# Kernel optimization log

Measured on AMD Instinct MI355X. Metric: run time of the kernel, lower is better.

The kernel has to match this reference:

```python
import jax, jax.numpy as jnp
import numpy as np

NUM_HEADS = 4
EPS = 1e-12  # torch F.normalize eps


def conv1x1(x, w):
    # x: (b,c,h,w), w: (co,ci,1,1) -> pointwise conv == channel GEMM
    return jnp.einsum('bchw,dc->bdhw', x, w[:, :, 0, 0])


def dwconv3x3(x, w):
    # depthwise 3x3, groups = channels; w: (c,1,3,3)
    c = x.shape[1]
    return jax.lax.conv_general_dilated(
        x, w, window_strides=(1, 1), padding=((1, 1), (1, 1)),
        dimension_numbers=('NCHW', 'OIHW', 'NCHW'), feature_group_count=c)


def l2_normalize(x, axis=-1):
    n = jnp.sqrt(jnp.sum(x * x, axis=axis, keepdims=True))
    return x / jnp.maximum(n, EPS)


def setup_inputs() -> dict:
    key = jax.random.key(0)
    ks = jax.random.split(key, 8)
    b, c, h, w = 4, 192, 128, 128
    s = 0.05
    return {
        'x': jax.random.normal(ks[0], (b, c, h, w), jnp.float32),
        'wq': jax.random.normal(ks[1], (c, c, 1, 1), jnp.float32) * s,
        'wq_dw': jax.random.normal(ks[2], (c, 1, 3, 3), jnp.float32) * s,
        'wk': jax.random.normal(ks[3], (c, c, 1, 1), jnp.float32) * s,
        'wk_dw': jax.random.normal(ks[4], (c, 1, 3, 3), jnp.float32) * s,
        'wv': jax.random.normal(ks[5], (c, c, 1, 1), jnp.float32) * s,
        'wv_dw': jax.random.normal(ks[6], (c, 1, 3, 3), jnp.float32) * s,
        'temperature': jnp.ones((NUM_HEADS, 1, 1), jnp.float32),
    }


def reference(x, wq, wq_dw, wk, wk_dw, wv, wv_dw, temperature):
    b, c, h, w = x.shape
    hd = NUM_HEADS
    ch = c // hd  # per-head channels
    n = h * w

    q = dwconv3x3(conv1x1(x, wq), wq_dw)
    k = dwconv3x3(conv1x1(x, wk), wk_dw)
    v = dwconv3x3(conv1x1(x, wv), wv_dw)

    # b (head c) h w -> b head c (h w)
    q = q.reshape(b, hd, ch, n)
    k = k.reshape(b, hd, ch, n)
    v = v.reshape(b, hd, ch, n)

    q = l2_normalize(q, axis=-1)
    k = l2_normalize(k, axis=-1)

    # channel-wise attention: (c x N) @ (N x c) -> (c x c)
    attn = jnp.einsum('bhcn,bhdn->bhcd', q, k) * temperature  # temperature: (head,1,1)
    attn = jax.nn.softmax(attn, axis=-1)
    out = jnp.einsum('bhcd,bhdn->bhcn', attn, v)
    return out.reshape(b, c, h, w)
```

## Files before the change

kernel.cpp:

```cpp
#include <hip/hip_runtime.h>
#include <hip/hip_bf16.h>


typedef __attribute__((ext_vector_type(8))) short short8;
typedef __attribute__((ext_vector_type(4))) float f32x4;

#define NB 4
#define NC 192
#define NN 16384
#define CH 48
#define NWELEM 115780

__device__ inline unsigned short f2bf(float f) {
  union { float f; unsigned int u; } c; c.f = f;
  unsigned int r = c.u + 0x7FFF + ((c.u >> 16) & 1);
  return (unsigned short)(r >> 16);
}
__device__ inline float bf2f(unsigned short u) {
  union { unsigned int u; float f; } c; c.u = ((unsigned int)u) << 16;
  return c.f;
}

__device__ inline bool detect_f32(const unsigned short* x) {
  int l = threadIdx.x & 63;
  unsigned short u = x[2 * (l * 997 + 1)];
  int e = (u >> 7) & 0xFF;
  bool extreme = (e < 90) || (e > 165);
  return __popcll(__ballot(extreme)) >= 8;
}

__global__ __launch_bounds__(256) void k_convert(const unsigned short* __restrict__ x,
                                                 const void* wq, const void* wk, const void* wv,
                                                 const void* wqd, const void* wkd, const void* wvd,
                                                 const void* temp,
                                                 unsigned short* __restrict__ canon) {
  bool f32 = detect_f32(x);
  int i = blockIdx.x * 256 + threadIdx.x;
  if (i >= NWELEM) return;
  const void* src; int off;
  if (i < 36864)       { src = wq;  off = i; }
  else if (i < 73728)  { src = wk;  off = i - 36864; }
  else if (i < 110592) { src = wv;  off = i - 73728; }
  else if (i < 112320) { src = wqd; off = i - 110592; }
  else if (i < 114048) { src = wkd; off = i - 112320; }
  else if (i < 115776) { src = wvd; off = i - 114048; }
  else                 { src = temp; off = i - 115776; }
  canon[i] = f32 ? f2bf(((const float*)src)[off])
                 : ((const unsigned short*)src)[off];
}

__global__ __launch_bounds__(256) void k_transpose(const unsigned short* __restrict__ X,
                                                   unsigned short* __restrict__ Xt) {
  __shared__ unsigned short tile[64 * 65];
  bool f32 = detect_f32(X);
  int b = blockIdx.z, c0 = blockIdx.y * 64, p0 = blockIdx.x * 64;
  int tid = threadIdx.x;
  if (f32) {
    const float* Xf = (const float*)X;
    for (int it = 0; it < 16; ++it) {
      int idx = it * 256 + tid;
      int c = idx >> 6, p = idx & 63;
      tile[c * 65 + p] = f2bf(Xf[((size_t)b * NC + c0 + c) * NN + p0 + p]);
    }
  } else {
    for (int it = 0; it < 16; ++it) {
      int idx = it * 256 + tid;
      int c = idx >> 6, p = idx & 63;
      tile[c * 65 + p] = X[((size_t)b * NC + c0 + c) * NN + p0 + p];
    }
  }
  __syncthreads();
  for (int it = 0; it < 2; ++it) {
    int idx = it * 256 + tid;
    int cc = idx & 7, p = idx >> 3;
    short8 v;
#pragma unroll
    for (int j = 0; j < 8; ++j) v[j] = (short)tile[(cc * 8 + j) * 65 + p];
    *(short8*)(Xt + ((size_t)b * NN + p0 + p) * NC + c0 + cc * 8) = v;
  }
}

#define LDP 200
__global__ __launch_bounds__(256) void k_conv1x1(const unsigned short* __restrict__ Wc,
                                                 const unsigned short* __restrict__ Xt,
                                                 unsigned short* __restrict__ Y) {
  __shared__ __align__(16) unsigned short Ws[64 * LDP];
  __shared__ __align__(16) unsigned short Xs[128 * LDP];
  int b = blockIdx.z, d0 = blockIdx.y * 64, p0 = blockIdx.x * 128;
  int tid = threadIdx.x;
  const unsigned short* tb = Xt + ((size_t)b * NN + p0) * NC;
  for (int it = 0; it < 12; ++it) {
    int idx = it * 256 + tid;
    short8 v = *(const short8*)(tb + idx * 8);
    int p = idx / 24, cc = idx % 24;
    *(short8*)(&Xs[p * LDP + cc * 8]) = v;
  }
  const unsigned short* wb = Wc + d0 * NC;
  for (int it = 0; it < 6; ++it) {
    int idx = it * 256 + tid;
    short8 v = *(const short8*)(wb + idx * 8);
    int d = idx / 24, cc = idx % 24;
    *(short8*)(&Ws[d * LDP + cc * 8]) = v;
  }
  __syncthreads();
  int lane = tid & 63, w = tid >> 6;
  int wm = w & 1, wn = w >> 1;
  int lrow = lane & 15, lq = lane >> 4;
  f32x4 acc[2][4];
  for (int mt = 0; mt < 2; ++mt)
    for (int nt = 0; nt < 4; ++nt) acc[mt][nt] = (f32x4){0.f, 0.f, 0.f, 0.f};
  for (int ks = 0; ks < 6; ++ks) {
    int k = ks * 32 + lq * 8;
    short8 a[2], bf[4];
    for (int mt = 0; mt < 2; ++mt)
      a[mt] = *(const short8*)(&Ws[(wm * 32 + mt * 16 + lrow) * LDP + k]);
    for (int nt = 0; nt < 4; ++nt)
      bf[nt] = *(const short8*)(&Xs[(wn * 64 + nt * 16 + lrow) * LDP + k]);
    for (int mt = 0; mt < 2; ++mt)
      for (int nt = 0; nt < 4; ++nt)
        acc[mt][nt] = __builtin_amdgcn_mfma_f32_16x16x32_bf16(a[mt], bf[nt], acc[mt][nt], 0, 0, 0);
  }
  for (int mt = 0; mt < 2; ++mt)
    for (int nt = 0; nt < 4; ++nt)
      for (int r = 0; r < 4; ++r) {
        int d = d0 + wm * 32 + mt * 16 + lq * 4 + r;
        int p = p0 + wn * 64 + nt * 16 + lrow;
        Y[((size_t)b * NC + d) * NN + p] = f2bf(acc[mt][nt][r]);
      }
}

__global__ __launch_bounds__(256) void k_dwconv(const unsigned short* __restrict__ Y,
                                                const unsigned short* __restrict__ Wdc,
                                                unsigned short* __restrict__ P,
                                                float* __restrict__ ss) {
  __shared__ float Ys[34][132];
  __shared__ float red[4];
  int b = blockIdx.z, c = blockIdx.y, r0 = blockIdx.x * 32;
  int tid = threadIdx.x;
  const unsigned short* base = Y + ((size_t)b * NC + c) * NN;
  for (int it = 0; it < 3; ++it) {
    int t = it * 256 + tid;
    if (t < 544) {
      int r = t >> 4, ch = t & 15;
      int gr = r0 - 1 + r;
      float f[8];
      if (gr >= 0 && gr < 128) {
        short8 v = *(const short8*)(base + gr * 128 + ch * 8);
#pragma unroll
        for (int j = 0; j < 8; ++j) f[j] = bf2f((unsigned short)v[j]);
      } else {
#pragma unroll
        for (int j = 0; j < 8; ++j) f[j] = 0.f;
      }
#pragma unroll
      for (int j2 = 0; j2 < 4; ++j2)
        *(float2*)(&Ys[r][2 + ch * 8 + 2 * j2]) = make_float2(f[2 * j2], f[2 * j2 + 1]);
    }
  }
  if (tid < 34) { Ys[tid][1] = 0.f; Ys[tid][130] = 0.f; }
  float wk9[9];
  for (int i = 0; i < 9; ++i) wk9[i] = bf2f(Wdc[c * 9 + i]);
  __syncthreads();
  float ssacc = 0.f;
  for (int it = 0; it < 2; ++it) {
    int t = it * 256 + tid;
    int r = t >> 4, ch = t & 15;
    float z[8];
#pragma unroll
    for (int j = 0; j < 8; ++j) z[j] = 0.f;
#pragma unroll
    for (int dy = 0; dy < 3; ++dy) {
      float row[10];
#pragma unroll
      for (int t2 = 0; t2 < 10; ++t2) row[t2] = Ys[r + dy][1 + ch * 8 + t2];
#pragma unroll
      for (int dx = 0; dx < 3; ++dx) {
        float wv = wk9[dy * 3 + dx];
#pragma unroll
        for (int j = 0; j < 8; ++j) z[j] += wv * row[j + dx];
      }
    }
    short8 sv;
#pragma unroll
    for (int j = 0; j < 8; ++j) { sv[j] = (short)f2bf(z[j]); ssacc += z[j] * z[j]; }
    *(short8*)(P + ((size_t)b * NC + c) * NN + (r0 + r) * 128 + ch * 8) = sv;
  }
  if (ss) {
    for (int off = 32; off; off >>= 1) ssacc += __shfl_down(ssacc, off);
    if ((tid & 63) == 0) red[tid >> 6] = ssacc;
    __syncthreads();
    if (tid == 0) atomicAdd(&ss[b * NC + c], red[0] + red[1] + red[2] + red[3]);
  }
}

__global__ __launch_bounds__(256) void k_attn(const unsigned short* __restrict__ Qp,
                                              const unsigned short* __restrict__ Kp,
                                              float* __restrict__ S) {
  __shared__ float Sred[CH * CH];
  int bh = blockIdx.y, chunk = blockIdx.x;
  int b = bh >> 2, h = bh & 3;
  int tid = threadIdx.x, lane = tid & 63, w = tid >> 6;
  int lrow = lane & 15, lq = lane >> 4;
  const unsigned short* Qb = Qp + ((size_t)b * NC + h * CH) * NN;
  const unsigned short* Kb = Kp + ((size_t)b * NC + h * CH) * NN;
  int nbase = chunk * 1024 + w * 256;
  f32x4 acc[3][3];
  for (int i = 0; i < 3; ++i)
    for (int j = 0; j < 3; ++j) acc[i][j] = (f32x4){0.f, 0.f, 0.f, 0.f};
  for (int ks = 0; ks < 8; ++ks) {
    int n = nbase + ks * 32 + lq * 8;
    short8 a[3], bb[3];
    for (int t = 0; t < 3; ++t) a[t]  = *(const short8*)(Qb + (size_t)(t * 16 + lrow) * NN + n);
    for (int t = 0; t < 3; ++t) bb[t] = *(const short8*)(Kb + (size_t)(t * 16 + lrow) * NN + n);
    for (int ti = 0; ti < 3; ++ti)
      for (int tj = 0; tj < 3; ++tj)
        acc[ti][tj] = __builtin_amdgcn_mfma_f32_16x16x32_bf16(a[ti], bb[tj], acc[ti][tj], 0, 0, 0);
  }
  for (int i = tid; i < CH * CH; i += 256) Sred[i] = 0.f;
  __syncthreads();
  for (int ti = 0; ti < 3; ++ti)
    for (int tj = 0; tj < 3; ++tj)
      for (int r = 0; r < 4; ++r) {
        int row = ti * 16 + lq * 4 + r, col = tj * 16 + lrow;
        atomicAdd(&Sred[row * CH + col], acc[ti][tj][r]);
      }
  __syncthreads();
  float* Sg = S + bh * (CH * CH);
  for (int i = tid; i < CH * CH; i += 256) atomicAdd(&Sg[i], Sred[i]);
}

__global__ void k_softmax(const float* __restrict__ S, const float* __restrict__ ssq,
                          const float* __restrict__ ssk, const unsigned short* __restrict__ tempc,
                          float* __restrict__ AT) {
  int bh = blockIdx.x, b = bh >> 2, h = bh & 3;
  int i = threadIdx.x;
  if (i >= CH) return;
  float t = bf2f(tempc[h]);
  float rq = 1.f / fmaxf(sqrtf(ssq[b * NC + h * CH + i]), 1e-12f);
  const float* Srow = S + bh * (CH * CH) + i * CH;
  float l[CH];
  float m = -1e30f;
  for (int j = 0; j < CH; ++j) {
    float rk = 1.f / fmaxf(sqrtf(ssk[b * NC + h * CH + j]), 1e-12f);
    l[j] = Srow[j] * rq * rk * t;
    m = fmaxf(m, l[j]);
  }
  float s = 0.f;
  for (int j = 0; j < CH; ++j) { l[j] = __expf(l[j] - m); s += l[j]; }
  float inv = 1.f / s;
  for (int j = 0; j < CH; ++j) AT[bh * (CH * CH) + j * CH + i] = l[j] * inv;
}

__global__ __launch_bounds__(256) void k_out(const float* __restrict__ AT,
                                             const unsigned short* __restrict__ Vp,
                                             void* __restrict__ Out,
                                             const unsigned short* __restrict__ x) {
  bool f32 = detect_f32(x);
  int bh = blockIdx.y, b = bh >> 2, h = bh & 3;
  int p0 = (blockIdx.x * 256 + threadIdx.x) * 2;
  const float* A = AT + bh * (CH * CH);
  const unsigned short* Vb = Vp + ((size_t)b * NC + h * CH) * NN;
  float a1[CH], a2[CH];
  for (int i = 0; i < CH; ++i) { a1[i] = 0.f; a2[i] = 0.f; }
  for (int j = 0; j < CH; ++j) {
    unsigned int u = *(const unsigned int*)(Vb + (size_t)j * NN + p0);
    float v1 = bf2f((unsigned short)(u & 0xFFFF));
    float v2 = bf2f((unsigned short)(u >> 16));
    const float* Aj = A + j * CH;
    for (int i = 0; i < CH; ++i) {
      float a = Aj[i];
      a1[i] += a * v1;
      a2[i] += a * v2;
    }
  }
  size_t obase = ((size_t)b * NC + h * CH) * NN;
  if (f32) {
    float* Of = (float*)Out;
    for (int i = 0; i < CH; ++i)
      *(float2*)(Of + obase + (size_t)i * NN + p0) = make_float2(a1[i], a2[i]);
  } else {
    unsigned short* Ob = (unsigned short*)Out;
    for (int i = 0; i < CH; ++i) {
      unsigned int u = ((unsigned int)f2bf(a2[i]) << 16) | f2bf(a1[i]);
      *(unsigned int*)(Ob + obase + (size_t)i * NN + p0) = u;
    }
  }
}

extern "C" void kernel_launch(void* const* d_in, const int* in_sizes, int n_in,
                              void* d_out, int out_size, void* d_ws, size_t ws_size,
                              hipStream_t stream) {
  const unsigned short* x = (const unsigned short*)d_in[0];

  const size_t TEN = (size_t)NB * NC * NN;
  unsigned short* bufA = (unsigned short*)d_ws;
  unsigned short* bufB = bufA + TEN;
  unsigned short* Xt   = bufB + TEN;
  float* ssq = (float*)(Xt + TEN);
  float* ssk = ssq + NB * NC;
  float* S   = ssk + NB * NC;
  float* AT  = S + 16 * CH * CH;
  unsigned short* canon = (unsigned short*)(AT + 16 * CH * CH);
  const unsigned short* Wq  = canon;
  const unsigned short* Wk  = canon + 36864;
  const unsigned short* Wv  = canon + 73728;
  const unsigned short* Wqd = canon + 110592;
  const unsigned short* Wkd = canon + 112320;
  const unsigned short* Wvd = canon + 114048;
  const unsigned short* Tmp = canon + 115776;

  hipMemsetAsync(ssq, 0, (2 * NB * NC + 16 * CH * CH) * sizeof(float), stream);
  k_convert<<<(NWELEM + 255) / 256, 256, 0, stream>>>(
      x, d_in[1], d_in[3], d_in[5], d_in[2], d_in[4], d_in[6], d_in[7], canon);
  k_transpose<<<dim3(NN / 64, NC / 64, NB), 256, 0, stream>>>(x, Xt);

  unsigned short* Ysc = (unsigned short*)d_out;

  k_conv1x1<<<dim3(NN / 128, NC / 64, NB), 256, 0, stream>>>(Wq, Xt, Ysc);
  k_dwconv<<<dim3(4, NC, NB), 256, 0, stream>>>(Ysc, Wqd, bufA, ssq);
  k_conv1x1<<<dim3(NN / 128, NC / 64, NB), 256, 0, stream>>>(Wk, Xt, Ysc);
  k_dwconv<<<dim3(4, NC, NB), 256, 0, stream>>>(Ysc, Wkd, bufB, ssk);
  k_attn<<<dim3(16, 16), 256, 0, stream>>>(bufA, bufB, S);
  k_softmax<<<16, 64, 0, stream>>>(S, ssq, ssk, Tmp, AT);
  k_conv1x1<<<dim3(NN / 128, NC / 64, NB), 256, 0, stream>>>(Wv, Xt, Ysc);
  k_dwconv<<<dim3(4, NC, NB), 256, 0, stream>>>(Ysc, Wvd, bufA, nullptr);
  k_out<<<dim3(NN / 512, 16), 256, 0, stream>>>(AT, bufA, d_out, x);
}
```

Baseline: 269.7 us.

## Fuse Q/K/V pointwise convs into one kernel and batch depthwise convs

```diff
diff --git a/kernel.cpp b/kernel.cpp
--- a/kernel.cpp
+++ b/kernel.cpp
@@ -10,6 +10,7 @@
 #define NN 16384
 #define CH 48
 #define NWELEM 115780
+#define NZERO 38400
 
 __device__ inline unsigned short f2bf(float f) {
   union { float f; unsigned int u; } c; c.f = f;
@@ -29,13 +30,20 @@
   return __popcll(__ballot(extreme)) >= 8;
 }
 
-__global__ __launch_bounds__(256) void k_convert(const unsigned short* __restrict__ x,
-                                                 const void* wq, const void* wk, const void* wv,
-                                                 const void* wqd, const void* wkd, const void* wvd,
-                                                 const void* temp,
-                                                 unsigned short* __restrict__ canon) {
+__global__ __launch_bounds__(256) void k_pre(const unsigned short* __restrict__ x,
+                                             const void* wq, const void* wk, const void* wv,
+                                             const void* wqd, const void* wkd, const void* wvd,
+                                             const void* temp,
+                                             unsigned short* __restrict__ canon,
+                                             float* __restrict__ zbase) {
+  int blk = blockIdx.x;
+  if (blk >= 453) {
+    int i = (blk - 453) * 256 + threadIdx.x;
+    if (i < NZERO) zbase[i] = 0.f;
+    return;
+  }
   bool f32 = detect_f32(x);
-  int i = blockIdx.x * 256 + threadIdx.x;
+  int i = blk * 256 + threadIdx.x;
   if (i >= NWELEM) return;
   const void* src; int off;
   if (i < 36864)       { src = wq;  off = i; }
@@ -81,12 +89,11 @@
 }
 
 #define LDP 200
-__global__ __launch_bounds__(256) void k_conv1x1(const unsigned short* __restrict__ Wc,
-                                                 const unsigned short* __restrict__ Xt,
-                                                 unsigned short* __restrict__ Y) {
-  __shared__ __align__(16) unsigned short Ws[64 * LDP];
+__global__ __launch_bounds__(256) void k_conv(const unsigned short* __restrict__ Wall,
+                                              const unsigned short* __restrict__ Xt,
+                                              unsigned short* __restrict__ Yall) {
   __shared__ __align__(16) unsigned short Xs[128 * LDP];
-  int b = blockIdx.z, d0 = blockIdx.y * 64, p0 = blockIdx.x * 128;
+  int b = blockIdx.y, p0 = blockIdx.x * 128;
   int tid = threadIdx.x;
   const unsigned short* tb = Xt + ((size_t)b * NN + p0) * NC;
   for (int it = 0; it < 12; ++it) {
@@ -95,49 +102,55 @@
     int p = idx / 24, cc = idx % 24;
     *(short8*)(&Xs[p * LDP + cc * 8]) = v;
   }
-  const unsigned short* wb = Wc + d0 * NC;
-  for (int it = 0; it < 6; ++it) {
-    int idx = it * 256 + tid;
-    short8 v = *(const short8*)(wb + idx * 8);
-    int d = idx / 24, cc = idx % 24;
-    *(short8*)(&Ws[d * LDP + cc * 8]) = v;
-  }
   __syncthreads();
   int lane = tid & 63, w = tid >> 6;
   int wm = w & 1, wn = w >> 1;
   int lrow = lane & 15, lq = lane >> 4;
-  f32x4 acc[2][4];
-  for (int mt = 0; mt < 2; ++mt)
-    for (int nt = 0; nt < 4; ++nt) acc[mt][nt] = (f32x4){0.f, 0.f, 0.f, 0.f};
-  for (int ks = 0; ks < 6; ++ks) {
-    int k = ks * 32 + lq * 8;
-    short8 a[2], bf[4];
+  short8 bf[6][4];
+  for (int ks = 0; ks < 6; ++ks)
+    for (int nt = 0; nt < 4; ++nt)
+      bf[ks][nt] = *(const short8*)(&Xs[(wn * 64 + nt * 16 + lrow) * LDP + ks * 32 + lq * 8]);
+  for (int dt = 0; dt < 9; ++dt) {
+    int d0 = dt * 64;
+    f32x4 acc[2][4];
     for (int mt = 0; mt < 2; ++mt)
-      a[mt] = *(const short8*)(&Ws[(wm * 32 + mt * 16 + lrow) * LDP + k]);
-    for (int nt = 0; nt < 4; ++nt)
-      bf[nt] = *(const short8*)(&Xs[(wn * 64 + nt * 16 + lrow) * LDP + k]);
+      for (int nt = 0; nt < 4; ++nt) acc[mt][nt] = (f32x4){0.f, 0.f, 0.f, 0.f};
+    for (int ks = 0; ks < 6; ++ks) {
+      int k = ks * 32 + lq * 8;
+      short8 a[2];
+      for (int mt = 0; mt < 2; ++mt)
+        a[mt] = *(const short8*)(Wall + (size_t)(d0 + wm * 32 + mt * 16 + lrow) * NC + k);
+      for (int mt = 0; mt < 2; ++mt)
+        for (int nt = 0; nt < 4; ++nt)
+          acc[mt][nt] = __builtin_amdgcn_mfma_f32_16x16x32_bf16(a[mt], bf[ks][nt], acc[mt][nt], 0, 0, 0);
+    }
+    int proj = dt / 3, c0 = (dt % 3) * 64;
+    unsigned short* Yb = Yall + (((size_t)proj * NB + b) * NC) * NN;
     for (int mt = 0; mt < 2; ++mt)
       for (int nt = 0; nt < 4; ++nt)
-        acc[mt][nt] = __builtin_amdgcn_mfma_f32_16x16x32_bf16(a[mt], bf[nt], acc[mt][nt], 0, 0, 0);
-  }
-  for (int mt = 0; mt < 2; ++mt)
-    for (int nt = 0; nt < 4; ++nt)
-      for (int r = 0; r < 4; ++r) {
-        int d = d0 + wm * 32 + mt * 16 + lq * 4 + r;
-        int p = p0 + wn * 64 + nt * 16 + lrow;
-        Y[((size_t)b * NC + d) * NN + p] = f2bf(acc[mt][nt][r]);
-      }
-}
-
-__global__ __launch_bounds__(256) void k_dwconv(const unsigned short* __restrict__ Y,
-                                                const unsigned short* __restrict__ Wdc,
-                                                unsigned short* __restrict__ P,
-                                                float* __restrict__ ss) {
+        for (int r = 0; r < 4; ++r) {
+          int c = c0 + wm * 32 + mt * 16 + lq * 4 + r;
+          int p = p0 + wn * 64 + nt * 16 + lrow;
+          Yb[(size_t)c * NN + p] = f2bf(acc[mt][nt][r]);
+        }
+  }
+}
+
+__global__ __launch_bounds__(256) void k_dwconv(const unsigned short* __restrict__ Yall,
+                                                const unsigned short* __restrict__ Wdall,
+                                                unsigned short* __restrict__ Pq,
+                                                unsigned short* __restrict__ Pk,
+                                                unsigned short* __restrict__ Pv,
+                                                float* __restrict__ ssq,
+                                                float* __restrict__ ssk) {
   __shared__ float Ys[34][132];
   __shared__ float red[4];
-  int b = blockIdx.z, c = blockIdx.y, r0 = blockIdx.x * 32;
+  int b = blockIdx.z, y = blockIdx.y, r0 = blockIdx.x * 32;
+  int proj = y / NC, c = y % NC;
   int tid = threadIdx.x;
-  const unsigned short* base = Y + ((size_t)b * NC + c) * NN;
+  const unsigned short* base = Yall + (((size_t)proj * NB + b) * NC + c) * NN;
+  unsigned short* P = (proj == 0 ? Pq : (proj == 1 ? Pk : Pv));
+  float* ss = (proj == 0 ? ssq : (proj == 1 ? ssk : nullptr));
   for (int it = 0; it < 3; ++it) {
     int t = it * 256 + tid;
     if (t < 544) {
@@ -159,7 +172,7 @@
   }
   if (tid < 34) { Ys[tid][1] = 0.f; Ys[tid][130] = 0.f; }
   float wk9[9];
-  for (int i = 0; i < 9; ++i) wk9[i] = bf2f(Wdc[c * 9 + i]);
+  for (int i = 0; i < 9; ++i) wk9[i] = bf2f(Wdall[(proj * NC + c) * 9 + i]);
   __syncthreads();
   float ssacc = 0.f;
   for (int it = 0; it < 2; ++it) {
@@ -295,34 +308,24 @@
   const size_t TEN = (size_t)NB * NC * NN;
   unsigned short* bufA = (unsigned short*)d_ws;
   unsigned short* bufB = bufA + TEN;
-  unsigned short* Xt   = bufB + TEN;
-  float* ssq = (float*)(Xt + TEN);
+  unsigned short* bufV = bufB + TEN;
+  unsigned short* Xt   = bufV + TEN;
+  unsigned short* Yall = Xt + TEN;
+  float* ssq = (float*)(Yall + 3 * TEN);
   float* ssk = ssq + NB * NC;
   float* S   = ssk + NB * NC;
   float* AT  = S + 16 * CH * CH;
   unsigned short* canon = (unsigned short*)(AT + 16 * CH * CH);
-  const unsigned short* Wq  = canon;
-  const unsigned short* Wk  = canon + 36864;
-  const unsigned short* Wv  = canon + 73728;
-  const unsigned short* Wqd = canon + 110592;
-  const unsigned short* Wkd = canon + 112320;
-  const unsigned short* Wvd = canon + 114048;
+  const unsigned short* Wall = canon;
+  const unsigned short* Wdall = canon + 110592;
   const unsigned short* Tmp = canon + 115776;
 
-  hipMemsetAsync(ssq, 0, (2 * NB * NC + 16 * CH * CH) * sizeof(float), stream);
-  k_convert<<<(NWELEM + 255) / 256, 256, 0, stream>>>(
-      x, d_in[1], d_in[3], d_in[5], d_in[2], d_in[4], d_in[6], d_in[7], canon);
+  k_pre<<<453 + (NZERO + 255) / 256, 256, 0, stream>>>(
+      x, d_in[1], d_in[3], d_in[5], d_in[2], d_in[4], d_in[6], d_in[7], canon, ssq);
   k_transpose<<<dim3(NN / 64, NC / 64, NB), 256, 0, stream>>>(x, Xt);
-
-  unsigned short* Ysc = (unsigned short*)d_out;
-
-  k_conv1x1<<<dim3(NN / 128, NC / 64, NB), 256, 0, stream>>>(Wq, Xt, Ysc);
-  k_dwconv<<<dim3(4, NC, NB), 256, 0, stream>>>(Ysc, Wqd, bufA, ssq);
-  k_conv1x1<<<dim3(NN / 128, NC / 64, NB), 256, 0, stream>>>(Wk, Xt, Ysc);
-  k_dwconv<<<dim3(4, NC, NB), 256, 0, stream>>>(Ysc, Wkd, bufB, ssk);
+  k_conv<<<dim3(NN / 128, NB), 256, 0, stream>>>(Wall, Xt, Yall);
+  k_dwconv<<<dim3(4, 3 * NC, NB), 256, 0, stream>>>(Yall, Wdall, bufA, bufB, bufV, ssq, ssk);
   k_attn<<<dim3(16, 16), 256, 0, stream>>>(bufA, bufB, S);
   k_softmax<<<16, 64, 0, stream>>>(S, ssq, ssk, Tmp, AT);
-  k_conv1x1<<<dim3(NN / 128, NC / 64, NB), 256, 0, stream>>>(Wv, Xt, Ysc);
-  k_dwconv<<<dim3(4, NC, NB), 256, 0, stream>>>(Ysc, Wvd, bufA, nullptr);
-  k_out<<<dim3(NN / 512, 16), 256, 0, stream>>>(AT, bufA, d_out, x);
-}
+  k_out<<<dim3(NN / 512, 16), 256, 0, stream>>>(AT, bufV, d_out, x);
+}
```

After: 258.5 us. 4.2% less time.
